# Kernel tuning notes

Measured on AMD Instinct MI355X. Metric: run time of the kernel, lower is better.

The kernel has to match this reference:

```python
import jax, jax.numpy as jnp
import numpy as np

DIM = 2048
THRESH = 0.33

def _ternary(w):
    # sign() with dead zone: {-1, 0, +1}; detached from grad (matches torch.no_grad)
    return jax.lax.stop_gradient(jnp.where(jnp.abs(w) < THRESH, 0.0, jnp.sign(w)))

def _bitlinear(x, w, b):
    # F.linear(x, ternary_w, bias): x @ ternary_w.T + b
    return jnp.einsum('bsd,od->bso', x, _ternary(w)) + b

def setup_inputs() -> dict:
    key = jax.random.key(0)
    ks = jax.random.split(key, 6)
    B, S, D = 8, 2048, DIM
    x = jax.random.normal(ks[0], (B, S, D), dtype=jnp.float32)
    h_prev = jax.random.normal(ks[1], (B, S, D), dtype=jnp.float32)
    # BitLinear reset_parameters: uniform(-1, 1); bias zeros
    wf = jax.random.uniform(ks[2], (D, D), minval=-1.0, maxval=1.0, dtype=jnp.float32)
    wc = jax.random.uniform(ks[3], (D, D), minval=-1.0, maxval=1.0, dtype=jnp.float32)
    wg = jax.random.uniform(ks[4], (D, D), minval=-1.0, maxval=1.0, dtype=jnp.float32)
    wo = jax.random.uniform(ks[5], (D, D), minval=-1.0, maxval=1.0, dtype=jnp.float32)
    bf = jnp.zeros((D,), dtype=jnp.float32)
    bc = jnp.zeros((D,), dtype=jnp.float32)
    bg = jnp.zeros((D,), dtype=jnp.float32)
    bo = jnp.zeros((D,), dtype=jnp.float32)
    return {"x": x, "h_prev": h_prev, "wf": wf, "bf": bf, "wc": wc, "bc": bc,
            "wg": wg, "bg": bg, "wo": wo, "bo": bo}

def reference(x, h_prev, wf, bf, wc, bc, wg, bg, wo, bo):
    f = jax.nn.sigmoid(_bitlinear(x, wf, bf))
    c = jax.nn.silu(_bitlinear(x, wc, bc))
    h = f * h_prev + (1.0 - f) * c
    g = jax.nn.sigmoid(_bitlinear(x, wg, bg))
    o = _bitlinear(g * h, wo, bo)
    return (o, h)
```

## Files before the change

### kernel.cpp

```cpp
#include <hip/hip_runtime.h>
#include <hip/hip_bf16.h>
#include <cstdint>

#define DIM   2048
#define MROWS 16384
#define NH    64

typedef __bf16 bf16x8 __attribute__((ext_vector_type(8)));
typedef float  f32x4  __attribute__((ext_vector_type(4)));
typedef unsigned short u16;
typedef unsigned int   u32;

#define BARRIER() asm volatile("s_barrier" ::: "memory")
#define WAITVM(N) asm volatile("s_waitcnt vmcnt(" #N ")" ::: "memory")


__device__ __forceinline__ u16 ternary_bits(float w) {
    u32 u = __float_as_uint(w);
    u16 s = (u16)((u >> 16) & 0x8000u);
    return (__builtin_fabsf(w) < 0.33f) ? (u16)0 : (u16)(0x3F80u | s);
}

__device__ __forceinline__ u16 f2bf_rne(float f) {
    u32 u = __float_as_uint(f);
    u32 r = (u + 0x7FFFu + ((u >> 16) & 1u)) >> 16;
    return (u16)r;
}

__device__ __forceinline__ void gload16(const void* g, void* l) {
    __builtin_amdgcn_global_load_lds(
        (const __attribute__((address_space(1))) void*)g,
        (__attribute__((address_space(3))) void*)l,
        16, 0, 0);
}


__global__ void prep_weights(const float* __restrict__ wf, const float* __restrict__ wc,
                             const float* __restrict__ wg, const float* __restrict__ wo,
                             u16* __restrict__ out) {
    const float* srcs[4] = {wf, wc, wg, wo};
    const float* src = srcs[blockIdx.y];
    u16* dst = out + (size_t)blockIdx.y * (DIM * DIM);
    int e = (blockIdx.x * 256 + threadIdx.x) * 8;
    float4 v0 = *(const float4*)(src + e);
    float4 v1 = *(const float4*)(src + e + 4);
    ushort4 o0, o1;
    o0.x = ternary_bits(v0.x); o0.y = ternary_bits(v0.y);
    o0.z = ternary_bits(v0.z); o0.w = ternary_bits(v0.w);
    o1.x = ternary_bits(v1.x); o1.y = ternary_bits(v1.y);
    o1.z = ternary_bits(v1.z); o1.w = ternary_bits(v1.w);
    *(ushort4*)(dst + e)     = o0;
    *(ushort4*)(dst + e + 4) = o1;
}

__global__ void cast_x(const float* __restrict__ x, u16* __restrict__ xb) {
    size_t e = ((size_t)blockIdx.x * 256 + threadIdx.x) * 8;
    float4 v0 = *(const float4*)(x + e);
    float4 v1 = *(const float4*)(x + e + 4);
    ushort4 o0, o1;
    o0.x = f2bf_rne(v0.x); o0.y = f2bf_rne(v0.y);
    o0.z = f2bf_rne(v0.z); o0.w = f2bf_rne(v0.w);
    o1.x = f2bf_rne(v1.x); o1.y = f2bf_rne(v1.y);
    o1.z = f2bf_rne(v1.z); o1.w = f2bf_rne(v1.w);
    *(ushort4*)(xb + e)     = o0;
    *(ushort4*)(xb + e + 4) = o1;
}


__global__ __launch_bounds__(512) void gemm1(
    const u16* __restrict__ xb,
    const u16* __restrict__ wt,
    const float* __restrict__ bfv_, const float* __restrict__ bcv_, const float* __restrict__ bgv_,
    const float* __restrict__ hprev,
    float* __restrict__ hout,
    u16* __restrict__ gh)
{
    __shared__ __align__(16) u16 lds[4][16384];

    const int tid  = threadIdx.x;
    const int lane = tid & 63;
    const int wave = tid >> 6;
    const int wr   = wave >> 2;
    const int wcq  = wave & 3;

    const int bid  = blockIdx.x;
    const int swz  = (bid & 7) * 256 + (bid >> 3);
    const int brow = (swz & 127) * 128;
    const int bcol = (swz >> 7) * 128;

    const int row512 = tid >> 2;
    const int gc4    = (tid & 3) ^ ((tid >> 3) & 3);
    const int ldst   = tid * 8;

    const int fr  = lane & 15;
    const int hi  = lane >> 4;
    const int csw = (hi ^ ((fr >> 1) & 3)) * 8;

    f32x4 acc0[3][4] = {};
    f32x4 acc1[3][4] = {};

    const u16* aSrc  = xb + (size_t)(brow + row512) * DIM;
    const u16* bSrc0 = wt + (size_t)(bcol + row512) * DIM;
    const size_t WST = (size_t)DIM * DIM;

    auto issueHalf = [&](int slot, int k0) {
        gload16(aSrc + k0 + gc4 * 8,                (u16*)&lds[slot][ldst]);
        gload16(bSrc0 + 0 * WST + k0 + gc4 * 8,     (u16*)&lds[slot][4096  + ldst]);
        gload16(bSrc0 + 1 * WST + k0 + gc4 * 8,     (u16*)&lds[slot][8192  + ldst]);
        gload16(bSrc0 + 2 * WST + k0 + gc4 * 8,     (u16*)&lds[slot][12288 + ldst]);
    };

    auto rdFrags = [&](const u16* sl, bf16x8 (&a)[4], bf16x8 (&b0)[3], bf16x8 (&b1)[3]) {
        #pragma unroll
        for (int mi = 0; mi < 4; ++mi)
            a[mi] = *(const bf16x8*)(sl + (wr * 64 + mi * 16 + fr) * 32 + csw);
        #pragma unroll
        for (int g = 0; g < 3; ++g)
            b0[g] = *(const bf16x8*)(sl + 4096 + g * 4096 + (wcq * 32 + fr) * 32 + csw);
        #pragma unroll
        for (int g = 0; g < 3; ++g)
            b1[g] = *(const bf16x8*)(sl + 4096 + g * 4096 + (wcq * 32 + 16 + fr) * 32 + csw);
    };

    auto cluster = [&](bf16x8 (&a)[4], bf16x8 (&b0)[3], bf16x8 (&b1)[3]) {
        __builtin_amdgcn_s_setprio(1);
        #pragma unroll
        for (int g = 0; g < 3; ++g)
            #pragma unroll
            for (int mi = 0; mi < 4; ++mi)
                acc0[g][mi] = __builtin_amdgcn_mfma_f32_16x16x32_bf16(a[mi], b0[g], acc0[g][mi], 0, 0, 0);
        #pragma unroll
        for (int g = 0; g < 3; ++g)
            #pragma unroll
            for (int mi = 0; mi < 4; ++mi)
                acc1[g][mi] = __builtin_amdgcn_mfma_f32_16x16x32_bf16(a[mi], b1[g], acc1[g][mi], 0, 0, 0);
        __builtin_amdgcn_s_setprio(0);
    };

    issueHalf(0, 0); issueHalf(1, 32); issueHalf(2, 64);
    WAITVM(8);
    BARRIER();

    bf16x8 a[4], b0[3], b1[3];
    #pragma unroll 1
    for (int j = 0; j < NH - 3; ++j) {
        const u16* sl = &lds[j & 3][0];
        issueHalf((j + 3) & 3, (j + 3) * 32);
        rdFrags(sl, a, b0, b1);
        WAITVM(8);
        BARRIER();
        cluster(a, b0, b1);
        BARRIER();
    }
    rdFrags(&lds[(NH - 3) & 3][0], a, b0, b1);
    WAITVM(4);
    BARRIER();
    cluster(a, b0, b1);
    BARRIER();
    rdFrags(&lds[(NH - 2) & 3][0], a, b0, b1);
    WAITVM(0);
    BARRIER();
    cluster(a, b0, b1);
    BARRIER();
    rdFrags(&lds[(NH - 1) & 3][0], a, b0, b1);
    cluster(a, b0, b1);

    auto epi = [&](int ni, f32x4 (&c)[3][4]) {
        const int col = bcol + wcq * 32 + ni * 16 + fr;
        const float bfv = bfv_[col], bcv = bcv_[col], bgv = bgv_[col];
        #pragma unroll
        for (int mi = 0; mi < 4; ++mi) {
            #pragma unroll
            for (int j = 0; j < 4; ++j) {
                const int row = brow + wr * 64 + mi * 16 + hi * 4 + j;
                const size_t idx = (size_t)row * DIM + col;
                float pf = c[0][mi][j] + bfv;
                float pc = c[1][mi][j] + bcv;
                float pg = c[2][mi][j] + bgv;
                float f  = 1.f / (1.f + __expf(-pf));
                float cc = pc / (1.f + __expf(-pc));
                float g  = 1.f / (1.f + __expf(-pg));
                float hh = f * hprev[idx] + (1.f - f) * cc;
                hout[idx] = hh;
                gh[idx] = f2bf_rne(g * hh);
            }
        }
    };
    epi(0, acc0);
    epi(1, acc1);
}


__global__ __launch_bounds__(512) void gemm2(
    const u16* __restrict__ gh,
    const u16* __restrict__ wot,
    const float* __restrict__ bov_,
    float* __restrict__ oout)
{
    __shared__ __align__(16) u16 lds[3 * 16384];

    const int tid  = threadIdx.x;
    const int lane = tid & 63;
    const int wave = tid >> 6;
    const int wr   = wave >> 2;
    const int wcq  = wave & 3;

    const int bid  = blockIdx.x;
    const int swz  = (bid & 7) * 64 + (bid >> 3);
    const int brow = (swz & 63) * 256;
    const int bcol = (swz >> 6) * 256;

    const int srow = tid >> 2;
    const int gc4  = (tid & 3) ^ ((tid >> 3) & 3);
    const int ldst = tid * 8;

    const int fr  = lane & 15;
    const int hi  = lane >> 4;
    const int csw = (hi ^ ((fr >> 1) & 3)) * 8;

    f32x4 accL[8][2] = {};
    f32x4 accH[8][2] = {};

    const u16* aSrc0 = gh  + (size_t)(brow + srow) * DIM;
    const u16* aSrc1 = gh  + (size_t)(brow + 128 + srow) * DIM;
    const u16* bSrc0 = wot + (size_t)(bcol + srow) * DIM;
    const u16* bSrc1 = wot + (size_t)(bcol + 128 + srow) * DIM;

    auto issueA = [&](int so, int k0) {
        gload16(aSrc0 + k0 + gc4 * 8, (u16*)&lds[so + ldst]);
        gload16(aSrc1 + k0 + gc4 * 8, (u16*)&lds[so + 4096 + ldst]);
    };
    auto issueB = [&](int so, int k0) {
        gload16(bSrc0 + k0 + gc4 * 8, (u16*)&lds[so + 8192 + ldst]);
        gload16(bSrc1 + k0 + gc4 * 8, (u16*)&lds[so + 12288 + ldst]);
    };

    auto rdA = [&](int so, bf16x8 (&a)[8]) {
        #pragma unroll
        for (int mi = 0; mi < 8; ++mi)
            a[mi] = *(const bf16x8*)(&lds[so + (wr * 128 + mi * 16 + fr) * 32 + csw]);
    };
    auto rdB2 = [&](int so, int nbase, bf16x8 (&b)[2]) {
        #pragma unroll
        for (int jn = 0; jn < 2; ++jn)
            b[jn] = *(const bf16x8*)(&lds[so + 8192 + (wcq * 64 + (nbase + jn) * 16 + fr) * 32 + csw]);
    };
    auto domfma2 = [&](bf16x8 (&a)[8], bf16x8 (&b)[2], f32x4 (&c)[8][2]) {
        __builtin_amdgcn_s_setprio(1);
        #pragma unroll
        for (int jn = 0; jn < 2; ++jn)
            #pragma unroll
            for (int mi = 0; mi < 8; ++mi)
                c[mi][jn] = __builtin_amdgcn_mfma_f32_16x16x32_bf16(a[mi], b[jn], c[mi][jn], 0, 0, 0);
        __builtin_amdgcn_s_setprio(0);
    };

    int so0 = 0, so1 = 16384, so2 = 32768;

    issueA(so0, 0); issueB(so0, 0);
    issueA(so1, 32); issueB(so1, 32);
    WAITVM(4);
    BARRIER();

    bf16x8 a[8], b[2];
    #pragma unroll 1
    for (int h = 0; h < NH - 2; ++h) {
        const int kn = (h + 2) * 32;
        rdA(so0, a); rdB2(so0, 0, b);
        issueA(so2, kn);
        BARRIER();
        domfma2(a, b, accL);
        BARRIER();
        rdB2(so0, 2, b);
        issueB(so2, kn);
        WAITVM(4);
        BARRIER();
        domfma2(a, b, accH);
        BARRIER();
        int t = so0; so0 = so1; so1 = so2; so2 = t;
    }
    rdA(so0, a); rdB2(so0, 0, b);
    BARRIER(); domfma2(a, b, accL); BARRIER();
    rdB2(so0, 2, b);
    WAITVM(0);
    BARRIER(); domfma2(a, b, accH); BARRIER();
    { int t = so0; so0 = so1; so1 = so2; so2 = t; }
    rdA(so0, a); rdB2(so0, 0, b);
    domfma2(a, b, accL);
    rdB2(so0, 2, b);
    domfma2(a, b, accH);

    auto epi2 = [&](int nbase, f32x4 (&c)[8][2]) {
        #pragma unroll
        for (int jn = 0; jn < 2; ++jn) {
            const int col = bcol + wcq * 64 + (nbase + jn) * 16 + fr;
            const float bov = bov_[col];
            #pragma unroll
            for (int mi = 0; mi < 8; ++mi)
                #pragma unroll
                for (int j = 0; j < 4; ++j)
                    oout[(size_t)(brow + wr * 128 + mi * 16 + hi * 4 + j) * DIM + col] = c[mi][jn][j] + bov;
        }
    };
    epi2(0, accL);
    epi2(2, accH);
}

extern "C" void kernel_launch(void* const* d_in, const int* in_sizes, int n_in,
                              void* d_out, int out_size, void* d_ws, size_t ws_size,
                              hipStream_t stream) {
    const float* x  = (const float*)d_in[0];
    const float* hp = (const float*)d_in[1];
    const float* wf = (const float*)d_in[2];
    const float* bf = (const float*)d_in[3];
    const float* wc = (const float*)d_in[4];
    const float* bc = (const float*)d_in[5];
    const float* wg = (const float*)d_in[6];
    const float* bg = (const float*)d_in[7];
    const float* wo = (const float*)d_in[8];
    const float* bo = (const float*)d_in[9];

    float* o_out = (float*)d_out;
    float* h_out = o_out + (size_t)MROWS * DIM;

    u16* w_t  = (u16*)d_ws;
    u16* x_bf = (u16*)((char*)d_ws + 33554432);
    u16* gh   = (u16*)((char*)d_ws + 100663296);

    prep_weights<<<dim3(2048, 4), 256, 0, stream>>>(wf, wc, wg, wo, w_t);
    cast_x<<<dim3(16384), 256, 0, stream>>>(x, x_bf);
    gemm1<<<dim3(2048), 512, 0, stream>>>(x_bf, w_t, bf, bc, bg, hp, h_out, gh);
    gemm2<<<dim3(512), 512, 0, stream>>>(gh, w_t + 3 * (size_t)DIM * DIM, bo, o_out);
}
```

Measured before the change: 722.1 us.

## Software-pipeline LDS fragment reads with MFMA in both GEMM kernels

Both GEMM main loops are restructured so that LDS fragment loads for the next k-step are issued while MFMAs for the current step run. A and B fragments are ping-ponged between two register sets, and the loop is unrolled by two so the sets can alternate. This is meant to hide LDS read latency behind matrix-core work and remove the read-then-compute serialization at each barrier. The cost is higher VGPR pressure from the duplicated fragment registers, which may reduce occupancy or cause spills. The second kernel also changes its wait count and barrier placement.

```diff
diff --git a/kernel.cpp b/kernel.cpp
--- a/kernel.cpp
+++ b/kernel.cpp
@@ -104,66 +104,93 @@
     const size_t WST = (size_t)DIM * DIM;
 
     auto issueHalf = [&](int slot, int k0) {
-        gload16(aSrc + k0 + gc4 * 8,                (u16*)&lds[slot][ldst]);
-        gload16(bSrc0 + 0 * WST + k0 + gc4 * 8,     (u16*)&lds[slot][4096  + ldst]);
-        gload16(bSrc0 + 1 * WST + k0 + gc4 * 8,     (u16*)&lds[slot][8192  + ldst]);
-        gload16(bSrc0 + 2 * WST + k0 + gc4 * 8,     (u16*)&lds[slot][12288 + ldst]);
-    };
-
-    auto rdFrags = [&](const u16* sl, bf16x8 (&a)[4], bf16x8 (&b0)[3], bf16x8 (&b1)[3]) {
+        gload16(aSrc + k0 + gc4 * 8,            (u16*)&lds[slot][ldst]);
+        gload16(bSrc0 + 0 * WST + k0 + gc4 * 8, (u16*)&lds[slot][4096  + ldst]);
+        gload16(bSrc0 + 1 * WST + k0 + gc4 * 8, (u16*)&lds[slot][8192  + ldst]);
+        gload16(bSrc0 + 2 * WST + k0 + gc4 * 8, (u16*)&lds[slot][12288 + ldst]);
+    };
+
+    auto rdA = [&](const u16* sl, bf16x8 (&a)[4]) {
         #pragma unroll
         for (int mi = 0; mi < 4; ++mi)
             a[mi] = *(const bf16x8*)(sl + (wr * 64 + mi * 16 + fr) * 32 + csw);
+    };
+    auto rdB0 = [&](const u16* sl, bf16x8 (&b)[3]) {
         #pragma unroll
         for (int g = 0; g < 3; ++g)
-            b0[g] = *(const bf16x8*)(sl + 4096 + g * 4096 + (wcq * 32 + fr) * 32 + csw);
+            b[g] = *(const bf16x8*)(sl + 4096 + g * 4096 + (wcq * 32 + fr) * 32 + csw);
+    };
+    auto rdB1 = [&](const u16* sl, bf16x8 (&b)[3]) {
         #pragma unroll
         for (int g = 0; g < 3; ++g)
-            b1[g] = *(const bf16x8*)(sl + 4096 + g * 4096 + (wcq * 32 + 16 + fr) * 32 + csw);
-    };
-
-    auto cluster = [&](bf16x8 (&a)[4], bf16x8 (&b0)[3], bf16x8 (&b1)[3]) {
+            b[g] = *(const bf16x8*)(sl + 4096 + g * 4096 + (wcq * 32 + 16 + fr) * 32 + csw);
+    };
+    auto mfmaC = [&](bf16x8 (&a)[4], bf16x8 (&b)[3], f32x4 (&c)[3][4]) {
         __builtin_amdgcn_s_setprio(1);
         #pragma unroll
         for (int g = 0; g < 3; ++g)
             #pragma unroll
             for (int mi = 0; mi < 4; ++mi)
-                acc0[g][mi] = __builtin_amdgcn_mfma_f32_16x16x32_bf16(a[mi], b0[g], acc0[g][mi], 0, 0, 0);
-        #pragma unroll
-        for (int g = 0; g < 3; ++g)
-            #pragma unroll
-            for (int mi = 0; mi < 4; ++mi)
-                acc1[g][mi] = __builtin_amdgcn_mfma_f32_16x16x32_bf16(a[mi], b1[g], acc1[g][mi], 0, 0, 0);
+                c[g][mi] = __builtin_amdgcn_mfma_f32_16x16x32_bf16(a[mi], b[g], c[g][mi], 0, 0, 0);
         __builtin_amdgcn_s_setprio(0);
     };
+
+    bf16x8 aP[4], b0P[3], aQ[4], b0Q[3], b1[3];
 
     issueHalf(0, 0); issueHalf(1, 32); issueHalf(2, 64);
     WAITVM(8);
     BARRIER();
-
-    bf16x8 a[4], b0[3], b1[3];
+    rdA(&lds[0][0], aP); rdB0(&lds[0][0], b0P);
+
+    auto step = [&](int j, bf16x8 (&aC)[4], bf16x8 (&b0C)[3],
+                    bf16x8 (&aN)[4], bf16x8 (&b0N)[3]) {
+        const u16* sl  = &lds[j & 3][0];
+        const u16* sln = &lds[(j + 1) & 3][0];
+        rdB1(sl, b1);
+        issueHalf((j + 3) & 3, (j + 3) * 32);
+        mfmaC(aC, b0C, acc0);
+        WAITVM(8);
+        BARRIER();
+        rdA(sln, aN); rdB0(sln, b0N);
+        mfmaC(aC, b1, acc1);
+        BARRIER();
+    };
+
     #pragma unroll 1
-    for (int j = 0; j < NH - 3; ++j) {
-        const u16* sl = &lds[j & 3][0];
-        issueHalf((j + 3) & 3, (j + 3) * 32);
-        rdFrags(sl, a, b0, b1);
-        WAITVM(8);
-        BARRIER();
-        cluster(a, b0, b1);
-        BARRIER();
-    }
-    rdFrags(&lds[(NH - 3) & 3][0], a, b0, b1);
-    WAITVM(4);
-    BARRIER();
-    cluster(a, b0, b1);
-    BARRIER();
-    rdFrags(&lds[(NH - 2) & 3][0], a, b0, b1);
-    WAITVM(0);
-    BARRIER();
-    cluster(a, b0, b1);
-    BARRIER();
-    rdFrags(&lds[(NH - 1) & 3][0], a, b0, b1);
-    cluster(a, b0, b1);
+    for (int j = 0; j < NH - 4; j += 2) {
+        step(j,     aP, b0P, aQ, b0Q);
+        step(j + 1, aQ, b0Q, aP, b0P);
+    }
+    step(NH - 4, aP, b0P, aQ, b0Q);
+
+    {
+        const u16* sl  = &lds[(NH - 3) & 3][0];
+        const u16* sln = &lds[(NH - 2) & 3][0];
+        rdB1(sl, b1);
+        mfmaC(aQ, b0Q, acc0);
+        WAITVM(4);
+        BARRIER();
+        rdA(sln, aP); rdB0(sln, b0P);
+        mfmaC(aQ, b1, acc1);
+        BARRIER();
+    }
+    {
+        const u16* sl  = &lds[(NH - 2) & 3][0];
+        const u16* sln = &lds[(NH - 1) & 3][0];
+        rdB1(sl, b1);
+        mfmaC(aP, b0P, acc0);
+        WAITVM(0);
+        BARRIER();
+        rdA(sln, aQ); rdB0(sln, b0Q);
+        mfmaC(aP, b1, acc1);
+        BARRIER();
+    }
+    {
+        const u16* sl = &lds[(NH - 1) & 3][0];
+        rdB1(sl, b1);
+        mfmaC(aQ, b0Q, acc0);
+        mfmaC(aQ, b1, acc1);
+    }
 
     auto epi = [&](int ni, f32x4 (&c)[3][4]) {
         const int col = bcol + wcq * 32 + ni * 16 + fr;
@@ -240,12 +267,17 @@
         for (int mi = 0; mi < 8; ++mi)
             a[mi] = *(const bf16x8*)(&lds[so + (wr * 128 + mi * 16 + fr) * 32 + csw]);
     };
-    auto rdB2 = [&](int so, int nbase, bf16x8 (&b)[2]) {
+    auto rdBL = [&](int so, bf16x8 (&b)[2]) {
         #pragma unroll
         for (int jn = 0; jn < 2; ++jn)
-            b[jn] = *(const bf16x8*)(&lds[so + 8192 + (wcq * 64 + (nbase + jn) * 16 + fr) * 32 + csw]);
-    };
-    auto domfma2 = [&](bf16x8 (&a)[8], bf16x8 (&b)[2], f32x4 (&c)[8][2]) {
+            b[jn] = *(const bf16x8*)(&lds[so + 8192 + (wcq * 64 + jn * 16 + fr) * 32 + csw]);
+    };
+    auto rdBH = [&](int so, bf16x8 (&b)[2]) {
+        #pragma unroll
+        for (int jn = 0; jn < 2; ++jn)
+            b[jn] = *(const bf16x8*)(&lds[so + 8192 + (wcq * 64 + (2 + jn) * 16 + fr) * 32 + csw]);
+    };
+    auto mfma2 = [&](bf16x8 (&a)[8], bf16x8 (&b)[2], f32x4 (&c)[8][2]) {
         __builtin_amdgcn_s_setprio(1);
         #pragma unroll
         for (int jn = 0; jn < 2; ++jn)
@@ -257,38 +289,49 @@
 
     int so0 = 0, so1 = 16384, so2 = 32768;
 
+    bf16x8 aP[8], bLP[2], aQ[8], bLQ[2], bH[2];
+
     issueA(so0, 0); issueB(so0, 0);
     issueA(so1, 32); issueB(so1, 32);
     WAITVM(4);
     BARRIER();
-
-    bf16x8 a[8], b[2];
+    rdA(so0, aP); rdBL(so0, bLP);
+
+    auto step = [&](int h, bf16x8 (&aC)[8], bf16x8 (&bLC)[2],
+                    bf16x8 (&aN)[8], bf16x8 (&bLN)[2]) {
+        const int kn = (h + 2) * 32;
+        rdBH(so0, bH);
+        issueA(so2, kn);
+        mfma2(aC, bLC, accL);
+        WAITVM(2);
+        BARRIER();
+        rdA(so1, aN); rdBL(so1, bLN);
+        issueB(so2, kn);
+        mfma2(aC, bH, accH);
+        BARRIER();
+        int t = so0; so0 = so1; so1 = so2; so2 = t;
+    };
+
     #pragma unroll 1
-    for (int h = 0; h < NH - 2; ++h) {
-        const int kn = (h + 2) * 32;
-        rdA(so0, a); rdB2(so0, 0, b);
-        issueA(so2, kn);
-        BARRIER();
-        domfma2(a, b, accL);
-        BARRIER();
-        rdB2(so0, 2, b);
-        issueB(so2, kn);
-        WAITVM(4);
-        BARRIER();
-        domfma2(a, b, accH);
+    for (int h = 0; h < NH - 2; h += 2) {
+        step(h,     aP, bLP, aQ, bLQ);
+        step(h + 1, aQ, bLQ, aP, bLP);
+    }
+    {
+        rdBH(so0, bH);
+        mfma2(aP, bLP, accL);
+        WAITVM(0);
+        BARRIER();
+        rdA(so1, aQ); rdBL(so1, bLQ);
+        mfma2(aP, bH, accH);
         BARRIER();
         int t = so0; so0 = so1; so1 = so2; so2 = t;
     }
-    rdA(so0, a); rdB2(so0, 0, b);
-    BARRIER(); domfma2(a, b, accL); BARRIER();
-    rdB2(so0, 2, b);
-    WAITVM(0);
-    BARRIER(); domfma2(a, b, accH); BARRIER();
-    { int t = so0; so0 = so1; so1 = so2; so2 = t; }
-    rdA(so0, a); rdB2(so0, 0, b);
-    domfma2(a, b, accL);
-    rdB2(so0, 2, b);
-    domfma2(a, b, accH);
+    {
+        rdBH(so0, bH);
+        mfma2(aQ, bLQ, accL);
+        mfma2(aQ, bH, accH);
+    }
 
     auto epi2 = [&](int nbase, f32x4 (&c)[8][2]) {
         #pragma unroll
```

Measured after the change: 715.1 us. About the same (-1.0%).
